# Kernel optimization log

Hardware: AMD Instinct MI355X
Metric: run time of the kernel (lower is better)

Reference implementation:

```python
import jax, jax.numpy as jnp
import numpy as np

B, N, C_IN, C_OUT = 128, 512, 64, 64
ALPHA = 0.2  # LeakyReLU negative slope
NEG_INF = -9e15


def setup_inputs() -> dict:
    key = jax.random.key(0)
    k_x, k_adj, k_W, k_a, k_b = jax.random.split(key, 5)
    x = jax.random.normal(k_x, (B, N, C_IN), dtype=jnp.float32)
    adj = jax.random.randint(k_adj, (N, N), 0, 2, dtype=jnp.int32)
    # Xavier-uniform-ish init for W:[2,C_IN,C_OUT] and a:[2*C_OUT,1]
    limW = 1.414 * np.sqrt(6.0 / (C_IN + C_OUT))
    W = jax.random.uniform(k_W, (2, C_IN, C_OUT), jnp.float32, -limW, limW)
    lima = 1.414 * np.sqrt(6.0 / (2 * C_OUT + 1))
    a = jax.random.uniform(k_a, (2 * C_OUT, 1), jnp.float32, -lima, lima)
    stdv = 1.0 / np.sqrt(C_OUT)
    bias = jax.random.uniform(k_b, (C_OUT,), jnp.float32, -stdv, stdv)
    return {"x": x, "adj": adj, "W": W, "a": a, "bias": bias}


def reference(x, adj, W, a, bias):
    F_out = W.shape[2]
    h0 = jnp.einsum('bnc,cf->bnf', x, W[0])
    h1 = jnp.einsum('bnc,cf->bnf', x, W[1])
    h = h0 + h1  # [B,N,F]
    # Separable additive attention score: e[b,i,j] = leaky(a1.h_i + a2.h_j)
    a1 = a[:F_out, 0]
    a2 = a[F_out:, 0]
    s1 = h @ a1  # [B,N]
    s2 = h @ a2  # [B,N]
    e = jax.nn.leaky_relu(s1[:, :, None] + s2[:, None, :], negative_slope=ALPHA)
    att = jnp.where(adj[None, :, :] > 0, e, NEG_INF)
    att = jax.nn.softmax(att, axis=2)  # [B,N,N]
    # attention*M (M=eye) picks diagonal -> route through h0; off-diagonal -> h1
    eye = jnp.eye(att.shape[1], dtype=att.dtype)
    diag = jnp.einsum('bii->bi', att)
    h_prime = diag[:, :, None] * h0 + jnp.einsum('bij,bjf->bif', att * (1.0 - eye), h1)
    return h_prime + bias
```

## Files before the change

### kernel.cpp

```cpp
#include <hip/hip_runtime.h>
#include <hip/hip_bf16.h>

#define BB 128
#define NN 512
#define ALPHA_ 0.2f
#define NEG_INF_ -9.0e15f
#define SPB 536
#define SXW 72

typedef short bf16x8 __attribute__((ext_vector_type(8)));
typedef float f32x4  __attribute__((ext_vector_type(4)));

__device__ __forceinline__ float bf2f(__hip_bfloat16 v) { return __bfloat162float(v); }

__global__ __launch_bounds__(256) void k0_bits(const int* __restrict__ adj,
                                               unsigned char* __restrict__ bits) {
    int idx = blockIdx.x * 256 + threadIdx.x;
    const int* p = adj + (size_t)idx * 8;
    unsigned m = 0;
    #pragma unroll
    for (int t = 0; t < 8; ++t) m |= (p[t] > 0 ? 1u : 0u) << t;
    bits[idx] = (unsigned char)m;
}

__global__ __launch_bounds__(256, 2) void k1_proj(
    const float* __restrict__ x, const float* __restrict__ W, const float* __restrict__ a,
    __hip_bfloat16* __restrict__ h1T, float* __restrict__ h0out,
    float* __restrict__ s1, float* __restrict__ s2)
{
    __shared__ __align__(16) unsigned short sX[64 * SXW];
    __shared__ __align__(16) unsigned short sWb[2][64 * SXW];
    __shared__ unsigned short sT[64 * 66];
    int tid = threadIdx.x, lane = tid & 63, w = tid >> 6;
    int lane15 = lane & 15, quad = lane >> 4;
    int b = blockIdx.x >> 3, n0 = (blockIdx.x & 7) << 6;

    for (int idx = tid; idx < 4096; idx += 256) {
        int c = idx >> 6, f = idx & 63;
        __hip_bfloat16 b0 = __float2bfloat16(W[idx]);
        __hip_bfloat16 b1 = __float2bfloat16(W[4096 + idx]);
        sWb[0][f * SXW + c] = *(unsigned short*)&b0;
        sWb[1][f * SXW + c] = *(unsigned short*)&b1;
    }
    {
        int nl = tid >> 2, q = tid & 3;
        const float* xp = x + ((size_t)b * NN + n0 + nl) * 64 + q * 16;
        float4 v0 = *(const float4*)(xp + 0);
        float4 v1 = *(const float4*)(xp + 4);
        float4 v2 = *(const float4*)(xp + 8);
        float4 v3 = *(const float4*)(xp + 12);
        union { bf16x8 v; __hip_bfloat16 h[8]; } pk0, pk1;
        pk0.h[0]=__float2bfloat16(v0.x); pk0.h[1]=__float2bfloat16(v0.y);
        pk0.h[2]=__float2bfloat16(v0.z); pk0.h[3]=__float2bfloat16(v0.w);
        pk0.h[4]=__float2bfloat16(v1.x); pk0.h[5]=__float2bfloat16(v1.y);
        pk0.h[6]=__float2bfloat16(v1.z); pk0.h[7]=__float2bfloat16(v1.w);
        pk1.h[0]=__float2bfloat16(v2.x); pk1.h[1]=__float2bfloat16(v2.y);
        pk1.h[2]=__float2bfloat16(v2.z); pk1.h[3]=__float2bfloat16(v2.w);
        pk1.h[4]=__float2bfloat16(v3.x); pk1.h[5]=__float2bfloat16(v3.y);
        pk1.h[6]=__float2bfloat16(v3.z); pk1.h[7]=__float2bfloat16(v3.w);
        *(bf16x8*)&sX[nl * SXW + q * 16]     = pk0.v;
        *(bf16x8*)&sX[nl * SXW + q * 16 + 8] = pk1.v;
    }
    __syncthreads();

    f32x4 acc0[4] = {{0,0,0,0},{0,0,0,0},{0,0,0,0},{0,0,0,0}};
    f32x4 acc1[4] = {{0,0,0,0},{0,0,0,0},{0,0,0,0},{0,0,0,0}};
    #pragma unroll
    for (int kt = 0; kt < 2; ++kt) {
        bf16x8 af = *(const bf16x8*)&sX[(w * 16 + lane15) * SXW + kt * 32 + quad * 8];
        #pragma unroll
        for (int nt = 0; nt < 4; ++nt) {
            bf16x8 b0 = *(const bf16x8*)&sWb[0][(nt * 16 + lane15) * SXW + kt * 32 + quad * 8];
            acc0[nt] = __builtin_amdgcn_mfma_f32_16x16x32_bf16(af, b0, acc0[nt], 0, 0, 0);
            bf16x8 b1 = *(const bf16x8*)&sWb[1][(nt * 16 + lane15) * SXW + kt * 32 + quad * 8];
            acc1[nt] = __builtin_amdgcn_mfma_f32_16x16x32_bf16(af, b1, acc1[nt], 0, 0, 0);
        }
    }

    float a1v[4], a2v[4];
    #pragma unroll
    for (int nt = 0; nt < 4; ++nt) {
        a1v[nt] = a[nt * 16 + lane15];
        a2v[nt] = a[64 + nt * 16 + lane15];
    }
    float p1[4] = {0, 0, 0, 0}, p2[4] = {0, 0, 0, 0};
    #pragma unroll
    for (int nt = 0; nt < 4; ++nt) {
        #pragma unroll
        for (int r = 0; r < 4; ++r) {
            int nl = w * 16 + quad * 4 + r;
            int f  = nt * 16 + lane15;
            float h0v = acc0[nt][r], h1v = acc1[nt][r];
            h0out[((size_t)b * NN + n0 + nl) * 64 + f] = h0v;
            __hip_bfloat16 hb = __float2bfloat16(h1v);
            sT[f * 66 + nl] = *(unsigned short*)&hb;
            float hs = h0v + h1v;
            p1[r] = fmaf(hs, a1v[nt], p1[r]);
            p2[r] = fmaf(hs, a2v[nt], p2[r]);
        }
    }
    #pragma unroll
    for (int r = 0; r < 4; ++r) {
        float v1 = p1[r], v2 = p2[r];
        #pragma unroll
        for (int o = 1; o < 16; o <<= 1) {
            v1 += __shfl_xor(v1, o, 64);
            v2 += __shfl_xor(v2, o, 64);
        }
        if (lane15 == 0) {
            int row = b * NN + n0 + w * 16 + quad * 4 + r;
            s1[row] = v1; s2[row] = v2;
        }
    }
    __syncthreads();
    unsigned short* h1Tu = (unsigned short*)h1T;
    #pragma unroll
    for (int fr = 0; fr < 16; ++fr) {
        int f = w * 16 + fr;
        h1Tu[(size_t)b * 32768 + f * 512 + n0 + lane] = sT[f * 66 + lane];
    }
}

__global__ __launch_bounds__(256, 2) void k2_att(
    const unsigned char* __restrict__ adjbits,
    const float* __restrict__ bias,
    const __hip_bfloat16* __restrict__ h1T,
    const float* __restrict__ s1, const float* __restrict__ s2,
    float* __restrict__ out)
{
    __shared__ __align__(16) __hip_bfloat16 sPb[32 * SPB];
    __shared__ float sInv[32];
    int tid = threadIdx.x, w = tid >> 6, lane = tid & 63;
    int b = blockIdx.y, i0 = blockIdx.x * 32;

    const float* s2b = s2 + (size_t)b * NN;
    float4 q0 = *(const float4*)(s2b + lane * 8);
    float4 q1 = *(const float4*)(s2b + lane * 8 + 4);
    float sv[8] = {q0.x, q0.y, q0.z, q0.w, q1.x, q1.y, q1.z, q1.w};

    for (int r2 = 0; r2 < 8; ++r2) {
        int r = 8 * w + r2;
        int i = i0 + r;
        float s1i = s1[(size_t)b * NN + i];
        unsigned mb = adjbits[(size_t)i * 64 + lane];
        float e[8];
        #pragma unroll
        for (int t = 0; t < 8; ++t) {
            float s = s1i + sv[t];
            s = fmaxf(s, ALPHA_ * s);
            e[t] = (mb & (1u << t)) ? s : NEG_INF_;
        }
        float lm = fmaxf(fmaxf(fmaxf(e[0], e[1]), fmaxf(e[2], e[3])),
                         fmaxf(fmaxf(e[4], e[5]), fmaxf(e[6], e[7])));
        #pragma unroll
        for (int o = 32; o > 0; o >>= 1) lm = fmaxf(lm, __shfl_xor(lm, o, 64));
        float p[8], ls = 0.f;
        #pragma unroll
        for (int t = 0; t < 8; ++t) { p[t] = __expf(e[t] - lm); ls += p[t]; }
        #pragma unroll
        for (int o = 32; o > 0; o >>= 1) ls += __shfl_xor(ls, o, 64);
        if (lane == 0) sInv[r] = 1.f / ls;
        union { bf16x8 v; __hip_bfloat16 h[8]; } pk;
        #pragma unroll
        for (int t = 0; t < 8; ++t) pk.h[t] = __float2bfloat16(p[t]);
        *(bf16x8*)&sPb[r * SPB + lane * 8] = pk.v;
    }
    __syncthreads();

    int lane15 = lane & 15, quad = lane >> 4;
    int n0w = w * 16;
    const __hip_bfloat16* h1b = h1T + (size_t)b * 32768;
    const __hip_bfloat16* bptr = h1b + (size_t)(n0w + lane15) * 512 + quad * 8;
    const __hip_bfloat16* aptr0 = &sPb[lane15 * SPB + quad * 8];
    const __hip_bfloat16* aptr1 = &sPb[(16 + lane15) * SPB + quad * 8];
    f32x4 acc0 = {0, 0, 0, 0}, acc1 = {0, 0, 0, 0};
    bf16x8 bfr[8];
    #pragma unroll
    for (int half = 0; half < 2; ++half) {
        #pragma unroll
        for (int g = 0; g < 8; ++g)
            bfr[g] = *(const bf16x8*)(bptr + (half * 8 + g) * 32);
        #pragma unroll
        for (int g = 0; g < 8; ++g) {
            int kt = half * 8 + g;
            bf16x8 a0 = *(const bf16x8*)(aptr0 + kt * 32);
            acc0 = __builtin_amdgcn_mfma_f32_16x16x32_bf16(a0, bfr[g], acc0, 0, 0, 0);
            bf16x8 a1 = *(const bf16x8*)(aptr1 + kt * 32);
            acc1 = __builtin_amdgcn_mfma_f32_16x16x32_bf16(a1, bfr[g], acc1, 0, 0, 0);
        }
    }

    int f = n0w + lane15;
    float biasf = bias[f];
    #pragma unroll
    for (int t = 0; t < 2; ++t) {
        f32x4 ac = t ? acc1 : acc0;
        #pragma unroll
        for (int r = 0; r < 4; ++r) {
            int m = t * 16 + quad * 4 + r;
            int i = i0 + m;
            size_t oidx = ((size_t)b * NN + i) * 64 + f;
            float hvi = bf2f(h1b[(size_t)f * 512 + i]);
            float pi  = bf2f(sPb[m * SPB + i]);
            float h0v = out[oidx];
            float inv = sInv[m];
            out[oidx] = (ac[r] - pi * hvi) * inv + pi * inv * h0v + biasf;
        }
    }
}

extern "C" void kernel_launch(void* const* d_in, const int* in_sizes, int n_in,
                              void* d_out, int out_size, void* d_ws, size_t ws_size,
                              hipStream_t stream) {
    const void* p_x = nullptr; const void* p_adj = nullptr; const void* p_W = nullptr;
    const void* p_a = nullptr; const void* p_bias = nullptr;
    for (int k = 0; k < n_in; ++k) {
        switch (in_sizes[k]) {
            case 128 * 512 * 64: p_x    = d_in[k]; break;
            case 512 * 512:      p_adj  = d_in[k]; break;
            case 2 * 64 * 64:    p_W    = d_in[k]; break;
            case 2 * 64:         p_a    = d_in[k]; break;
            case 64:             p_bias = d_in[k]; break;
        }
    }
    const float* x    = (const float*)p_x;
    const int*   adj  = (const int*)p_adj;
    const float* W    = (const float*)p_W;
    const float* a    = (const float*)p_a;
    const float* bias = (const float*)p_bias;
    float* out = (float*)d_out;

    __hip_bfloat16* h1T = (__hip_bfloat16*)d_ws;
    float* s1 = (float*)((char*)d_ws + (8u << 20));
    float* s2 = s1 + 65536;
    unsigned char* adjbits = (unsigned char*)(s2 + 65536);

    k0_bits<<<dim3(128), 256, 0, stream>>>(adj, adjbits);
    k1_proj<<<dim3(BB * 8), 256, 0, stream>>>(x, W, a, h1T, out, s1, s2);
    k2_att<<<dim3(NN / 32, BB), 256, 0, stream>>>(adjbits, bias, h1T, s1, s2, out);
}
```

Measured before the change: 117.2 us.

## Precast W once in prep kernel, load MFMA fragments directly, drop diagonal gather

The W-to-bf16 transposed conversion moves out of every k1 block into the prep kernel, which runs once. k1 now loads W fragments and x rows straight from global memory into registers, so it no longer needs its shared-memory staging or the barrier before the matrix multiply. In k2 the diagonal probability is saved to shared memory and zeroed before the bf16 pack, which removes the scattered h1T gather and subtraction in the epilogue. The costs are more register pressure in k1, uncoalesced per-lane x loads, and a slight precision change because the diagonal is no longer subtracted after bf16 rounding.

```diff
diff --git a/kernel.cpp b/kernel.cpp
--- a/kernel.cpp
+++ b/kernel.cpp
@@ -6,74 +6,69 @@
 #define ALPHA_ 0.2f
 #define NEG_INF_ -9.0e15f
 #define SPB 536
-#define SXW 72
 
 typedef short bf16x8 __attribute__((ext_vector_type(8)));
 typedef float f32x4  __attribute__((ext_vector_type(4)));
 
 __device__ __forceinline__ float bf2f(__hip_bfloat16 v) { return __bfloat162float(v); }
 
-__global__ __launch_bounds__(256) void k0_bits(const int* __restrict__ adj,
-                                               unsigned char* __restrict__ bits) {
-    int idx = blockIdx.x * 256 + threadIdx.x;
-    const int* p = adj + (size_t)idx * 8;
-    unsigned m = 0;
-    #pragma unroll
-    for (int t = 0; t < 8; ++t) m |= (p[t] > 0 ? 1u : 0u) << t;
-    bits[idx] = (unsigned char)m;
+__global__ __launch_bounds__(256) void k0_prep(const int* __restrict__ adj,
+                                               const float* __restrict__ W,
+                                               unsigned char* __restrict__ bits,
+                                               unsigned short* __restrict__ Wb) {
+    if (blockIdx.x < 128) {
+        int idx = blockIdx.x * 256 + threadIdx.x;
+        const int* p = adj + (size_t)idx * 8;
+        unsigned m = 0;
+        #pragma unroll
+        for (int t = 0; t < 8; ++t) m |= (p[t] > 0 ? 1u : 0u) << t;
+        bits[idx] = (unsigned char)m;
+    } else {
+        int gid = (blockIdx.x - 128) * 256 + threadIdx.x;
+        int mat = gid >> 12, rem = gid & 4095;
+        int f = rem >> 6, c = rem & 63;
+        __hip_bfloat16 v = __float2bfloat16(W[mat * 4096 + c * 64 + f]);
+        Wb[mat * 4096 + f * 64 + c] = *(unsigned short*)&v;
+    }
 }
 
 __global__ __launch_bounds__(256, 2) void k1_proj(
-    const float* __restrict__ x, const float* __restrict__ W, const float* __restrict__ a,
+    const float* __restrict__ x, const unsigned short* __restrict__ Wb,
+    const float* __restrict__ a,
     __hip_bfloat16* __restrict__ h1T, float* __restrict__ h0out,
     float* __restrict__ s1, float* __restrict__ s2)
 {
-    __shared__ __align__(16) unsigned short sX[64 * SXW];
-    __shared__ __align__(16) unsigned short sWb[2][64 * SXW];
     __shared__ unsigned short sT[64 * 66];
     int tid = threadIdx.x, lane = tid & 63, w = tid >> 6;
     int lane15 = lane & 15, quad = lane >> 4;
     int b = blockIdx.x >> 3, n0 = (blockIdx.x & 7) << 6;
 
-    for (int idx = tid; idx < 4096; idx += 256) {
-        int c = idx >> 6, f = idx & 63;
-        __hip_bfloat16 b0 = __float2bfloat16(W[idx]);
-        __hip_bfloat16 b1 = __float2bfloat16(W[4096 + idx]);
-        sWb[0][f * SXW + c] = *(unsigned short*)&b0;
-        sWb[1][f * SXW + c] = *(unsigned short*)&b1;
-    }
-    {
-        int nl = tid >> 2, q = tid & 3;
-        const float* xp = x + ((size_t)b * NN + n0 + nl) * 64 + q * 16;
+    bf16x8 bfr[2][4][2];
+    #pragma unroll
+    for (int mat = 0; mat < 2; ++mat)
+        #pragma unroll
+        for (int nt = 0; nt < 4; ++nt)
+            #pragma unroll
+            for (int kt = 0; kt < 2; ++kt)
+                bfr[mat][nt][kt] = *(const bf16x8*)(Wb + mat * 4096 + (nt * 16 + lane15) * 64 + kt * 32 + quad * 8);
+
+    int myrow = b * NN + n0 + w * 16 + lane15;
+    f32x4 acc0[4] = {{0,0,0,0},{0,0,0,0},{0,0,0,0},{0,0,0,0}};
+    f32x4 acc1[4] = {{0,0,0,0},{0,0,0,0},{0,0,0,0},{0,0,0,0}};
+    #pragma unroll
+    for (int kt = 0; kt < 2; ++kt) {
+        const float* xp = x + (size_t)myrow * 64 + kt * 32 + quad * 8;
         float4 v0 = *(const float4*)(xp + 0);
         float4 v1 = *(const float4*)(xp + 4);
-        float4 v2 = *(const float4*)(xp + 8);
-        float4 v3 = *(const float4*)(xp + 12);
-        union { bf16x8 v; __hip_bfloat16 h[8]; } pk0, pk1;
-        pk0.h[0]=__float2bfloat16(v0.x); pk0.h[1]=__float2bfloat16(v0.y);
-        pk0.h[2]=__float2bfloat16(v0.z); pk0.h[3]=__float2bfloat16(v0.w);
-        pk0.h[4]=__float2bfloat16(v1.x); pk0.h[5]=__float2bfloat16(v1.y);
-        pk0.h[6]=__float2bfloat16(v1.z); pk0.h[7]=__float2bfloat16(v1.w);
-        pk1.h[0]=__float2bfloat16(v2.x); pk1.h[1]=__float2bfloat16(v2.y);
-        pk1.h[2]=__float2bfloat16(v2.z); pk1.h[3]=__float2bfloat16(v2.w);
-        pk1.h[4]=__float2bfloat16(v3.x); pk1.h[5]=__float2bfloat16(v3.y);
-        pk1.h[6]=__float2bfloat16(v3.z); pk1.h[7]=__float2bfloat16(v3.w);
-        *(bf16x8*)&sX[nl * SXW + q * 16]     = pk0.v;
-        *(bf16x8*)&sX[nl * SXW + q * 16 + 8] = pk1.v;
-    }
-    __syncthreads();
-
-    f32x4 acc0[4] = {{0,0,0,0},{0,0,0,0},{0,0,0,0},{0,0,0,0}};
-    f32x4 acc1[4] = {{0,0,0,0},{0,0,0,0},{0,0,0,0},{0,0,0,0}};
-    #pragma unroll
-    for (int kt = 0; kt < 2; ++kt) {
-        bf16x8 af = *(const bf16x8*)&sX[(w * 16 + lane15) * SXW + kt * 32 + quad * 8];
+        union { bf16x8 v; __hip_bfloat16 h[8]; } af;
+        af.h[0] = __float2bfloat16(v0.x); af.h[1] = __float2bfloat16(v0.y);
+        af.h[2] = __float2bfloat16(v0.z); af.h[3] = __float2bfloat16(v0.w);
+        af.h[4] = __float2bfloat16(v1.x); af.h[5] = __float2bfloat16(v1.y);
+        af.h[6] = __float2bfloat16(v1.z); af.h[7] = __float2bfloat16(v1.w);
         #pragma unroll
         for (int nt = 0; nt < 4; ++nt) {
-            bf16x8 b0 = *(const bf16x8*)&sWb[0][(nt * 16 + lane15) * SXW + kt * 32 + quad * 8];
-            acc0[nt] = __builtin_amdgcn_mfma_f32_16x16x32_bf16(af, b0, acc0[nt], 0, 0, 0);
-            bf16x8 b1 = *(const bf16x8*)&sWb[1][(nt * 16 + lane15) * SXW + kt * 32 + quad * 8];
-            acc1[nt] = __builtin_amdgcn_mfma_f32_16x16x32_bf16(af, b1, acc1[nt], 0, 0, 0);
+            acc0[nt] = __builtin_amdgcn_mfma_f32_16x16x32_bf16(af.v, bfr[0][nt][kt], acc0[nt], 0, 0, 0);
+            acc1[nt] = __builtin_amdgcn_mfma_f32_16x16x32_bf16(af.v, bfr[1][nt][kt], acc1[nt], 0, 0, 0);
         }
     }
 
@@ -129,7 +124,7 @@
     float* __restrict__ out)
 {
     __shared__ __align__(16) __hip_bfloat16 sPb[32 * SPB];
-    __shared__ float sInv[32];
+    __shared__ float sInv[32], sPi[32];
     int tid = threadIdx.x, w = tid >> 6, lane = tid & 63;
     int b = blockIdx.y, i0 = blockIdx.x * 32;
 
@@ -160,6 +155,10 @@
         #pragma unroll
         for (int o = 32; o > 0; o >>= 1) ls += __shfl_xor(ls, o, 64);
         if (lane == 0) sInv[r] = 1.f / ls;
+        if ((i >> 3) == lane) {
+            sPi[r] = p[i & 7];
+            p[i & 7] = 0.f;
+        }
         union { bf16x8 v; __hip_bfloat16 h[8]; } pk;
         #pragma unroll
         for (int t = 0; t < 8; ++t) pk.h[t] = __float2bfloat16(p[t]);
@@ -200,11 +199,9 @@
             int m = t * 16 + quad * 4 + r;
             int i = i0 + m;
             size_t oidx = ((size_t)b * NN + i) * 64 + f;
-            float hvi = bf2f(h1b[(size_t)f * 512 + i]);
-            float pi  = bf2f(sPb[m * SPB + i]);
             float h0v = out[oidx];
-            float inv = sInv[m];
-            out[oidx] = (ac[r] - pi * hvi) * inv + pi * inv * h0v + biasf;
+            float inv = sInv[m], pi = sPi[m];
+            out[oidx] = ac[r] * inv + pi * inv * h0v + biasf;
         }
     }
 }
@@ -234,8 +231,9 @@
     float* s1 = (float*)((char*)d_ws + (8u << 20));
     float* s2 = s1 + 65536;
     unsigned char* adjbits = (unsigned char*)(s2 + 65536);
-
-    k0_bits<<<dim3(128), 256, 0, stream>>>(adj, adjbits);
-    k1_proj<<<dim3(BB * 8), 256, 0, stream>>>(x, W, a, h1T, out, s1, s2);
+    unsigned short* Wb = (unsigned short*)(adjbits + 32768);
+
+    k0_prep<<<dim3(160), 256, 0, stream>>>(adj, W, adjbits, Wb);
+    k1_proj<<<dim3(BB * 8), 256, 0, stream>>>(x, Wb, a, h1T, out, s1, s2);
     k2_att<<<dim3(NN / 32, BB), 256, 0, stream>>>(adjbits, bias, h1T, s1, s2, out);
 }
```

Result: slower. 120.8 us (+3.1%).
